# Kernel optimization log

Measured on AMD Instinct MI355X. Metric: run time of the kernel, lower is better.

The kernel has to match this reference:

```python
import jax, jax.numpy as jnp
import numpy as np
import math

B, S, E, H, DFF = 8, 1024, 1024, 16, 4096
DK = E // H
EPS = 1e-6


def _layernorm(x, alpha, bias):
    # Faithful to the torch module: uses unbiased std (ddof=1) and divides by (std + eps)
    mean = jnp.mean(x, axis=-1, keepdims=True)
    var = jnp.sum((x - mean) ** 2, axis=-1, keepdims=True) / (x.shape[-1] - 1)
    std = jnp.sqrt(var)
    return alpha * (x - mean) / (std + EPS) + bias


def setup_inputs() -> dict:
    key = jax.random.key(0)
    ks = jax.random.split(key, 16)
    sc_e = 1.0 / math.sqrt(E)
    sc_f = 1.0 / math.sqrt(DFF)
    inp = {
        "x": jax.random.normal(ks[0], (B, S, E), dtype=jnp.float32),
        "mask": jnp.ones((1, 1, S, S), dtype=jnp.int32),
        # linear weights stored as (in, out)
        "wq": jax.random.normal(ks[1], (E, E), jnp.float32) * sc_e,
        "bq": jnp.zeros((E,), jnp.float32),
        "wk": jax.random.normal(ks[2], (E, E), jnp.float32) * sc_e,
        "bk": jnp.zeros((E,), jnp.float32),
        "wv": jax.random.normal(ks[3], (E, E), jnp.float32) * sc_e,
        "bv": jnp.zeros((E,), jnp.float32),
        "wo": jax.random.normal(ks[4], (E, E), jnp.float32) * sc_e,
        "bo": jnp.zeros((E,), jnp.float32),
        "w1": jax.random.normal(ks[5], (E, DFF), jnp.float32) * sc_e,
        "b1": jnp.zeros((DFF,), jnp.float32),
        "w2": jax.random.normal(ks[6], (DFF, E), jnp.float32) * sc_f,
        "b2": jnp.zeros((E,), jnp.float32),
        "ln1_a": jnp.ones((E,), jnp.float32),
        "ln1_b": jnp.zeros((E,), jnp.float32),
        "ln2_a": jnp.ones((E,), jnp.float32),
        "ln2_b": jnp.zeros((E,), jnp.float32),
    }
    return inp


def _mha(x, mask, wq, bq, wk, bk, wv, bv, wo, bo):
    q = (x @ wq + bq).reshape(B, S, H, DK).transpose(0, 2, 1, 3)  # [B,H,S,DK]
    k = (x @ wk + bk).reshape(B, S, H, DK).transpose(0, 2, 1, 3)
    v = (x @ wv + bv).reshape(B, S, H, DK).transpose(0, 2, 1, 3)
    scores = jnp.einsum("bhqd,bhkd->bhqk", q, k) / math.sqrt(DK)  # [B,H,S,S]
    scores = jnp.where(mask == 0, jnp.float32(-1e9), scores)
    attn = jax.nn.softmax(scores, axis=-1)
    out = jnp.einsum("bhqk,bhkd->bhqd", attn, v)  # [B,H,S,DK]
    out = out.transpose(0, 2, 1, 3).reshape(B, S, E)
    return out @ wo + bo


def reference(x, mask, wq, bq, wk, bk, wv, bv, wo, bo, w1, b1, w2, b2,
              ln1_a, ln1_b, ln2_a, ln2_b):
    # Residual connection 1 (pre-norm): x + dropout(attn(norm(x))) ; dropout=0 at eval
    h1 = x + _mha(_layernorm(x, ln1_a, ln1_b), mask, wq, bq, wk, bk, wv, bv, wo, bo)
    # Residual connection 2: h1 + ffn(norm(h1))
    n2 = _layernorm(h1, ln2_a, ln2_b)
    ff = jax.nn.relu(n2 @ w1 + b1) @ w2 + b2
    return h1 + ff
```

## Files before the change

### kernel.cpp

```cpp
#include <hip/hip_runtime.h>
#include <hip/hip_bf16.h>
#include <cstdint>
#include <cstddef>

#define BB   8
#define SS   1024
#define EE   1024
#define HH   16
#define DKK  64
#define DFFN 4096
#define NROWS (BB*SS)

typedef __attribute__((ext_vector_type(8))) short short8;
typedef __attribute__((ext_vector_type(4))) short s16x4;
typedef __attribute__((ext_vector_type(4))) float f32x4;

__device__ __forceinline__ short f2bf(float f) {
  __hip_bfloat16 h = __float2bfloat16(f);
  return __builtin_bit_cast(short, h);
}

__device__ __forceinline__ void gload_lds16(const void* g, void* l) {
  __builtin_amdgcn_global_load_lds((const __attribute__((address_space(1))) void*)g,
                                   (__attribute__((address_space(3))) void*)l, 16, 0, 0);
}

__device__ __forceinline__ f32x4 mfma16(s16x4 a, s16x4 b, f32x4 c) {
#if __has_builtin(__builtin_amdgcn_mfma_f32_16x16x16_bf16)
  return __builtin_amdgcn_mfma_f32_16x16x16_bf16(a, b, c, 0, 0, 0);
#elif __has_builtin(__builtin_amdgcn_mfma_f32_16x16x16bf16_1k)
  return __builtin_amdgcn_mfma_f32_16x16x16bf16_1k(a, b, c, 0, 0, 0);
#else
  f32x4 d = c;
  asm("v_mfma_f32_16x16x16_bf16 %0, %1, %2, %0" : "+v"(d) : "v"(a), "v"(b));
  return d;
#endif
}

__global__ __launch_bounds__(256) void wtrans_kernel(const float* __restrict__ in,
                                                     short* __restrict__ out,
                                                     int R, int C) {
  __shared__ float tile[32][33];
  int c0 = blockIdx.x * 32, r0 = blockIdx.y * 32;
  int tx = threadIdx.x, ty = threadIdx.y;
#pragma unroll
  for (int i = 0; i < 32; i += 8)
    tile[ty + i][tx] = in[(size_t)(r0 + ty + i) * C + (c0 + tx)];
  __syncthreads();
#pragma unroll
  for (int i = 0; i < 32; i += 8)
    out[(size_t)(c0 + ty + i) * R + (r0 + tx)] = f2bf(tile[tx][ty + i]);
}

__global__ __launch_bounds__(256) void ln_kernel(const float* __restrict__ x,
                                                 const float* __restrict__ alpha,
                                                 const float* __restrict__ beta,
                                                 short* __restrict__ out) {
  __shared__ float sbuf[4];
  int row = blockIdx.x;
  int tid = threadIdx.x;
  const float* xr = x + (size_t)row * EE;
  float4 v = reinterpret_cast<const float4*>(xr)[tid];
  float s = v.x + v.y + v.z + v.w;
#pragma unroll
  for (int o = 32; o > 0; o >>= 1) s += __shfl_down(s, o);
  if ((tid & 63) == 0) sbuf[tid >> 6] = s;
  __syncthreads();
  float mean = (sbuf[0] + sbuf[1] + sbuf[2] + sbuf[3]) * (1.0f / EE);
  __syncthreads();
  float dx = v.x - mean, dy = v.y - mean, dz = v.z - mean, dw = v.w - mean;
  float sq = dx * dx + dy * dy + dz * dz + dw * dw;
#pragma unroll
  for (int o = 32; o > 0; o >>= 1) sq += __shfl_down(sq, o);
  if ((tid & 63) == 0) sbuf[tid >> 6] = sq;
  __syncthreads();
  float var = (sbuf[0] + sbuf[1] + sbuf[2] + sbuf[3]) * (1.0f / (EE - 1));
  float inv = 1.0f / (sqrtf(var) + 1e-6f);
  float4 a = reinterpret_cast<const float4*>(alpha)[tid];
  float4 b = reinterpret_cast<const float4*>(beta)[tid];
  size_t base = (size_t)row * EE + tid * 4;
  out[base + 0] = f2bf(a.x * dx * inv + b.x);
  out[base + 1] = f2bf(a.y * dy * inv + b.y);
  out[base + 2] = f2bf(a.z * dz * inv + b.z);
  out[base + 3] = f2bf(a.w * dw * inv + b.w);
}

template <int EPI>
__global__ __launch_bounds__(256, 4) void gemm_bt(const short* __restrict__ A,
                                                  const short* __restrict__ Bt,
                                                  const float* __restrict__ bias,
                                                  const float* __restrict__ resid,
                                                  void* __restrict__ out,
                                                  int N, int K, int NTN) {
  __shared__ short As[2][4096];
  __shared__ short Bs[2][4096];
  int tid = threadIdx.x;
  int lane = tid & 63, w = tid >> 6;
  int wr = w >> 1, wc = w & 1;
  int g = lane >> 4, c = lane & 15;

  int nwg = gridDim.x;
  int wg = blockIdx.x;
  int swg = (wg & 7) * (nwg >> 3) + (wg >> 3);
  int mt = swg / NTN, nt = swg % NTN;
  int m0 = mt * 128, n0 = nt * 128;

  int r0 = tid >> 2;
  int gslot = (tid & 3) ^ ((r0 >> 1) & 3);
  const short* pA = A + (size_t)(m0 + r0) * K + gslot * 8;
  const short* pB = Bt + (size_t)(n0 + r0) * K + gslot * 8;
  const size_t row64 = (size_t)64 * K;

  f32x4 acc[4][4] = {};

#define STAGE(B, T)                                                             \
  {                                                                             \
    gload_lds16(pA + (size_t)(T) * 32,         (char*)As[B] + w * 1024);        \
    gload_lds16(pA + (size_t)(T) * 32 + row64, (char*)As[B] + 4096 + w * 1024); \
    gload_lds16(pB + (size_t)(T) * 32,         (char*)Bs[B] + w * 1024);        \
    gload_lds16(pB + (size_t)(T) * 32 + row64, (char*)Bs[B] + 4096 + w * 1024); \
  }

  int NKT = K >> 5;
  STAGE(0, 0);
  __syncthreads();
  int buf = 0;

  int so = (g ^ ((c >> 1) & 3)) * 8;

  for (int t = 0; t < NKT; ++t) {
    if (t + 1 < NKT) STAGE(buf ^ 1, t + 1);

    short8 af[4], bfr[4];
#pragma unroll
    for (int i = 0; i < 4; ++i) {
      af[i]  = *(const short8*)&As[buf][(wr * 64 + i * 16 + c) * 32 + so];
      bfr[i] = *(const short8*)&Bs[buf][(wc * 64 + i * 16 + c) * 32 + so];
    }
    __builtin_amdgcn_s_setprio(1);
#pragma unroll
    for (int mi = 0; mi < 4; ++mi)
#pragma unroll
      for (int nf = 0; nf < 4; ++nf)
        acc[mi][nf] = __builtin_amdgcn_mfma_f32_16x16x32_bf16(af[mi], bfr[nf], acc[mi][nf], 0, 0, 0);
    __builtin_amdgcn_s_setprio(0);
    __syncthreads();
    buf ^= 1;
  }
#undef STAGE

  int rb_ = m0 + wr * 64;
  int cb_ = n0 + wc * 64;
#pragma unroll
  for (int mi = 0; mi < 4; ++mi) {
#pragma unroll
    for (int nf = 0; nf < 4; ++nf) {
      int col = cb_ + nf * 16 + c;
      float bv = bias[col];
      if (EPI == 5) {
        int which = col >> 10;
        int inner = col & 1023;
        int h = inner >> 6, d = inner & 63;
        if (which < 2) {
          short* dst = (short*)out + (size_t)which * (8u * 1024 * 1024);
#pragma unroll
          for (int j = 0; j < 4; ++j) {
            int row = rb_ + mi * 16 + g * 4 + j;
            int b = row >> 10, s = row & 1023;
            dst[(((size_t)(b * HH + h)) * SS + s) * DKK + d] = f2bf(acc[mi][nf][j] + bv);
          }
        } else {
          int row0 = rb_ + mi * 16 + g * 4;
          int b = row0 >> 10, s0 = row0 & 1023;
          s16x4 pkv;
#pragma unroll
          for (int j = 0; j < 4; ++j) pkv[j] = f2bf(acc[mi][nf][j] + bv);
          *(s16x4*)((short*)out + 2u * 8 * 1024 * 1024 +
                    (((size_t)(b * HH + h)) * DKK + d) * SS + s0) = pkv;
        }
      } else {
#pragma unroll
        for (int j = 0; j < 4; ++j) {
          int row = rb_ + mi * 16 + g * 4 + j;
          float val = acc[mi][nf][j] + bv;
          if (EPI == 1) {
            ((short*)out)[(size_t)row * N + col] = f2bf(val > 0.f ? val : 0.f);
          } else {
            ((float*)out)[(size_t)row * N + col] = resid[(size_t)row * N + col] + val;
          }
        }
      }
    }
  }
}

__global__ __launch_bounds__(256, 3) void attn_kernel(const short* __restrict__ q,
                                                      const short* __restrict__ k,
                                                      const short* __restrict__ vt,
                                                      short* __restrict__ out) {
  __shared__ short Ks[2][64 * 64];
  __shared__ short Vs[2][64 * 64];
  int bh = blockIdx.x, qt = blockIdx.y;
  int tid = threadIdx.x, lane = tid & 63, w = tid >> 6;
  int g = lane >> 4, c = lane & 15;
  const short* qp = q + (size_t)bh * SS * DKK;
  const short* kp = k + (size_t)bh * SS * DKK;
  const short* vp = vt + (size_t)bh * DKK * SS;

  int q0 = qt * 128 + w * 32;

  short8 qf[2][2];
#pragma unroll
  for (int qb = 0; qb < 2; ++qb)
#pragma unroll
    for (int ks = 0; ks < 2; ++ks)
      qf[qb][ks] = *(const short8*)(qp + (size_t)(q0 + qb * 16 + c) * DKK + ks * 32 + g * 8);

  f32x4 oacc[2][4];
#pragma unroll
  for (int qb = 0; qb < 2; ++qb)
#pragma unroll
    for (int nd = 0; nd < 4; ++nd)
#pragma unroll
      for (int j = 0; j < 4; ++j) oacc[qb][nd][j] = 0.f;
  float mrun[2] = {-1e30f, -1e30f}, lrun[2] = {0.f, 0.f};

  int rs = lane >> 3;
  int cs = lane & 7;
  int swz = (cs ^ rs) * 8;

  int buf = 0;
#define STAGE(B, T)                                                                  \
  {                                                                                  \
    _Pragma("unroll")                                                                \
    for (int cc = 0; cc < 2; ++cc) {                                                 \
      int chunk = w * 2 + cc;                                                        \
      int row = chunk * 8 + rs;                                                      \
      gload_lds16(kp + (size_t)((T) * 64 + row) * DKK + swz, &Ks[B][chunk * 512]);   \
      gload_lds16(vp + (size_t)row * SS + (T) * 64 + swz, &Vs[B][chunk * 512]);      \
    }                                                                                \
  }

  STAGE(0, 0);
  __syncthreads();

  for (int t = 0; t < SS / 64; ++t) {
    if (t < SS / 64 - 1) STAGE(buf ^ 1, t + 1);

    f32x4 sc[2][4];
#pragma unroll
    for (int qb = 0; qb < 2; ++qb)
#pragma unroll
      for (int nf = 0; nf < 4; ++nf)
#pragma unroll
        for (int j = 0; j < 4; ++j) sc[qb][nf][j] = 0.f;
#pragma unroll
    for (int ks = 0; ks < 2; ++ks) {
      short8 kf[4];
#pragma unroll
      for (int nf = 0; nf < 4; ++nf) {
        int row = nf * 16 + c;
        int off = row * 64 + (((ks * 64 + g * 16) ^ ((c & 7) << 4)) >> 1);
        kf[nf] = *(const short8*)&Ks[buf][off];
      }
#pragma unroll
      for (int qb = 0; qb < 2; ++qb)
#pragma unroll
        for (int nf = 0; nf < 4; ++nf)
          sc[qb][nf] = __builtin_amdgcn_mfma_f32_16x16x32_bf16(kf[nf], qf[qb][ks], sc[qb][nf], 0, 0, 0);
    }

    s16x4 pk[2][4];
    float corr[2];
#pragma unroll
    for (int qb = 0; qb < 2; ++qb) {
      float pm = -1e30f;
#pragma unroll
      for (int nf = 0; nf < 4; ++nf)
#pragma unroll
        for (int j = 0; j < 4; ++j) pm = fmaxf(pm, sc[qb][nf][j]);
      pm = fmaxf(pm, __shfl_xor(pm, 16));
      pm = fmaxf(pm, __shfl_xor(pm, 32));
      pm *= 0.125f;
      float mnew = fmaxf(mrun[qb], pm);
      corr[qb] = __expf(mrun[qb] - mnew);
      mrun[qb] = mnew;
      float rsum = 0.f;
#pragma unroll
      for (int nf = 0; nf < 4; ++nf) {
        float p0 = __expf(sc[qb][nf][0] * 0.125f - mnew);
        float p1 = __expf(sc[qb][nf][1] * 0.125f - mnew);
        float p2 = __expf(sc[qb][nf][2] * 0.125f - mnew);
        float p3 = __expf(sc[qb][nf][3] * 0.125f - mnew);
        rsum += (p0 + p1) + (p2 + p3);
        pk[qb][nf][0] = f2bf(p0); pk[qb][nf][1] = f2bf(p1);
        pk[qb][nf][2] = f2bf(p2); pk[qb][nf][3] = f2bf(p3);
      }
      rsum += __shfl_xor(rsum, 16);
      rsum += __shfl_xor(rsum, 32);
      lrun[qb] = lrun[qb] * corr[qb] + rsum;
    }
#pragma unroll
    for (int qb = 0; qb < 2; ++qb) {
      float cj[4];
#pragma unroll
      for (int j = 0; j < 4; ++j) cj[j] = __shfl(corr[qb], (lane & 48) | (g * 4 + j));
#pragma unroll
      for (int nd = 0; nd < 4; ++nd)
#pragma unroll
        for (int j = 0; j < 4; ++j) oacc[qb][nd][j] *= cj[j];
    }

#pragma unroll
    for (int nf = 0; nf < 4; ++nf) {
      s16x4 vf[4];
#pragma unroll
      for (int nd = 0; nd < 4; ++nd) {
        int row = nd * 16 + c;
        int off = row * 64 + (((nf * 32 + g * 8) ^ ((c & 7) << 4)) >> 1);
        vf[nd] = *(const s16x4*)&Vs[buf][off];
      }
#pragma unroll
      for (int qb = 0; qb < 2; ++qb)
#pragma unroll
        for (int nd = 0; nd < 4; ++nd)
          oacc[qb][nd] = mfma16(pk[qb][nf], vf[nd], oacc[qb][nd]);
    }
    __syncthreads();
    buf ^= 1;
  }
#undef STAGE

  int b = bh >> 4, h = bh & 15;
#pragma unroll
  for (int qb = 0; qb < 2; ++qb) {
#pragma unroll
    for (int j = 0; j < 4; ++j) {
      float linv = 1.0f / __shfl(lrun[qb], (lane & 48) | (g * 4 + j));
      int srow = q0 + qb * 16 + g * 4 + j;
#pragma unroll
      for (int nd = 0; nd < 4; ++nd)
        out[((size_t)b * SS + srow) * EE + h * DKK + nd * 16 + c] = f2bf(oacc[qb][nd][j] * linv);
    }
  }
}

extern "C" void kernel_launch(void* const* d_in, const int* in_sizes, int n_in,
                              void* d_out, int out_size, void* d_ws, size_t ws_size,
                              hipStream_t stream) {
  (void)in_sizes; (void)n_in; (void)out_size; (void)ws_size;
  const float* x   = (const float*)d_in[0];
  const float* wq  = (const float*)d_in[2];  const float* bq  = (const float*)d_in[3];
  const float* wk  = (const float*)d_in[4];  const float* bk  = (const float*)d_in[5];
  const float* wv  = (const float*)d_in[6];  const float* bv  = (const float*)d_in[7];
  const float* wo  = (const float*)d_in[8];  const float* bo  = (const float*)d_in[9];
  const float* w1  = (const float*)d_in[10]; const float* b1  = (const float*)d_in[11];
  const float* w2  = (const float*)d_in[12]; const float* b2  = (const float*)d_in[13];
  const float* l1a = (const float*)d_in[14]; const float* l1b = (const float*)d_in[15];
  const float* l2a = (const float*)d_in[16]; const float* l2b = (const float*)d_in[17];
  float* out = (float*)d_out;

  char* ws = (char*)d_ws;
  const size_t MB = 1024ull * 1024ull;
  short* wqkvT = (short*)(ws + 0 * MB);
  short* woT = (short*)(ws + 6 * MB);
  short* w1T = (short*)(ws + 8 * MB);
  short* w2T = (short*)(ws + 16 * MB);
  short* n1  = (short*)(ws + 24 * MB);
  short* qb  = (short*)(ws + 40 * MB);
  short* ff1 = (short*)(ws + 40 * MB);
  short* ao  = (short*)(ws + 88 * MB);
  float* bqkv = (float*)(ws + 100 * MB);
  float* h1  = (float*)(ws + 104 * MB);

  hipMemcpyAsync(bqkv,        bq, EE * sizeof(float), hipMemcpyDeviceToDevice, stream);
  hipMemcpyAsync(bqkv + EE,   bk, EE * sizeof(float), hipMemcpyDeviceToDevice, stream);
  hipMemcpyAsync(bqkv + 2*EE, bv, EE * sizeof(float), hipMemcpyDeviceToDevice, stream);

  dim3 tb(32, 8);
  wtrans_kernel<<<dim3(EE / 32, EE / 32), tb, 0, stream>>>(wq, wqkvT, EE, EE);
  wtrans_kernel<<<dim3(EE / 32, EE / 32), tb, 0, stream>>>(wk, wqkvT + 1024 * 1024, EE, EE);
  wtrans_kernel<<<dim3(EE / 32, EE / 32), tb, 0, stream>>>(wv, wqkvT + 2 * 1024 * 1024, EE, EE);
  wtrans_kernel<<<dim3(EE / 32, EE / 32), tb, 0, stream>>>(wo, woT, EE, EE);
  wtrans_kernel<<<dim3(DFFN / 32, EE / 32), tb, 0, stream>>>(w1, w1T, EE, DFFN);
  wtrans_kernel<<<dim3(EE / 32, DFFN / 32), tb, 0, stream>>>(w2, w2T, DFFN, EE);

  ln_kernel<<<NROWS, 256, 0, stream>>>(x, l1a, l1b, n1);

  gemm_bt<5><<<dim3(64 * 24), 256, 0, stream>>>(n1, wqkvT, bqkv, nullptr, qb, 3072, EE, 24);

  attn_kernel<<<dim3(BB * HH, SS / 128), 256, 0, stream>>>(qb, qb + 8 * 1024 * 1024,
                                                           qb + 16 * 1024 * 1024, ao);

  gemm_bt<2><<<dim3(64 * 8), 256, 0, stream>>>(ao, woT, bo, x, h1, EE, EE, 8);

  ln_kernel<<<NROWS, 256, 0, stream>>>(h1, l2a, l2b, n1);

  gemm_bt<1><<<dim3(64 * 32), 256, 0, stream>>>(n1, w1T, b1, nullptr, ff1, DFFN, EE, 32);
  gemm_bt<2><<<dim3(64 * 8), 256, 0, stream>>>(ff1, w2T, b2, h1, out, EE, DFFN, 8);
}
```

Baseline: 404.2 us.

## Triple-buffer GEMM LDS staging with manual waitcnt and one barrier per tile

Replaces the double-buffered LDS pipeline in the bf16 GEMM kernel with a three-slot ring. Two K tiles are prefetched ahead, and each iteration loads fragments from the current slot, issues the next global-to-LDS loads, then waits with explicit vmcnt/lgkmcnt counts and a single barrier before the MFMAs. The goal is to hide more global load latency behind compute and remove the trailing __syncthreads. In exchange it raises LDS use per block by half and lowers the launch-bounds occupancy hint from 4 to 3, which may reduce waves per CU.

```diff
diff --git a/kernel.cpp b/kernel.cpp
--- a/kernel.cpp
+++ b/kernel.cpp
@@ -86,14 +86,14 @@
 }
 
 template <int EPI>
-__global__ __launch_bounds__(256, 4) void gemm_bt(const short* __restrict__ A,
+__global__ __launch_bounds__(256, 3) void gemm_bt(const short* __restrict__ A,
                                                   const short* __restrict__ Bt,
                                                   const float* __restrict__ bias,
                                                   const float* __restrict__ resid,
                                                   void* __restrict__ out,
                                                   int N, int K, int NTN) {
-  __shared__ short As[2][4096];
-  __shared__ short Bs[2][4096];
+  __shared__ short As[3][4096];
+  __shared__ short Bs[3][4096];
   int tid = threadIdx.x;
   int lane = tid & 63, w = tid >> 6;
   int wr = w >> 1, wc = w & 1;
@@ -113,41 +113,72 @@
 
   f32x4 acc[4][4] = {};
 
-#define STAGE(B, T)                                                             \
-  {                                                                             \
-    gload_lds16(pA + (size_t)(T) * 32,         (char*)As[B] + w * 1024);        \
-    gload_lds16(pA + (size_t)(T) * 32 + row64, (char*)As[B] + 4096 + w * 1024); \
-    gload_lds16(pB + (size_t)(T) * 32,         (char*)Bs[B] + w * 1024);        \
-    gload_lds16(pB + (size_t)(T) * 32 + row64, (char*)Bs[B] + 4096 + w * 1024); \
+#define STAGE(SL, T)                                                                \
+  {                                                                                 \
+    gload_lds16(pA + (size_t)(T) * 32,         (char*)As[SL] + w * 1024);           \
+    gload_lds16(pA + (size_t)(T) * 32 + row64, (char*)As[SL] + 4096 + w * 1024);    \
+    gload_lds16(pB + (size_t)(T) * 32,         (char*)Bs[SL] + w * 1024);           \
+    gload_lds16(pB + (size_t)(T) * 32 + row64, (char*)Bs[SL] + 4096 + w * 1024);    \
+  }
+
+  int so = (g ^ ((c >> 1) & 3)) * 8;
+  int raA = (wr * 64 + c) * 32 + so;
+  int raB = (wc * 64 + c) * 32 + so;
+
+  short8 af[4], bfr[4];
+
+#define FRAGS(SL)                                                \
+  {                                                              \
+    _Pragma("unroll") for (int i = 0; i < 4; ++i) {              \
+      af[i]  = *(const short8*)&As[SL][raA + i * 512];           \
+      bfr[i] = *(const short8*)&Bs[SL][raB + i * 512];           \
+    }                                                            \
+  }
+
+#define MFMAS                                                                        \
+  {                                                                                  \
+    __builtin_amdgcn_s_setprio(1);                                                   \
+    _Pragma("unroll") for (int mi = 0; mi < 4; ++mi)                                 \
+        _Pragma("unroll") for (int nf = 0; nf < 4; ++nf)                             \
+            acc[mi][nf] = __builtin_amdgcn_mfma_f32_16x16x32_bf16(af[mi], bfr[nf],   \
+                                                                  acc[mi][nf], 0, 0, 0); \
+    __builtin_amdgcn_s_setprio(0);                                                   \
   }
 
   int NKT = K >> 5;
+
   STAGE(0, 0);
-  __syncthreads();
-  int buf = 0;
-
-  int so = (g ^ ((c >> 1) & 3)) * 8;
-
-  for (int t = 0; t < NKT; ++t) {
-    if (t + 1 < NKT) STAGE(buf ^ 1, t + 1);
-
-    short8 af[4], bfr[4];
-#pragma unroll
-    for (int i = 0; i < 4; ++i) {
-      af[i]  = *(const short8*)&As[buf][(wr * 64 + i * 16 + c) * 32 + so];
-      bfr[i] = *(const short8*)&Bs[buf][(wc * 64 + i * 16 + c) * 32 + so];
-    }
-    __builtin_amdgcn_s_setprio(1);
-#pragma unroll
-    for (int mi = 0; mi < 4; ++mi)
-#pragma unroll
-      for (int nf = 0; nf < 4; ++nf)
-        acc[mi][nf] = __builtin_amdgcn_mfma_f32_16x16x32_bf16(af[mi], bfr[nf], acc[mi][nf], 0, 0, 0);
-    __builtin_amdgcn_s_setprio(0);
-    __syncthreads();
-    buf ^= 1;
-  }
+  STAGE(1, 1);
+  asm volatile("s_waitcnt vmcnt(4)" ::: "memory");
+  __builtin_amdgcn_s_barrier();
+
+  int cur = 0;
+  for (int t = 0; t < NKT - 2; ++t) {
+    int nxt = cur + 2; if (nxt >= 3) nxt -= 3;
+    FRAGS(cur);
+    STAGE(nxt, t + 2);
+    asm volatile("s_waitcnt lgkmcnt(0)" ::: "memory");
+    asm volatile("s_waitcnt vmcnt(4)" ::: "memory");
+    __builtin_amdgcn_s_barrier();
+    __builtin_amdgcn_sched_barrier(0);
+    MFMAS;
+    ++cur; if (cur >= 3) cur -= 3;
+  }
+  FRAGS(cur);
+  asm volatile("s_waitcnt lgkmcnt(0)" ::: "memory");
+  asm volatile("s_waitcnt vmcnt(0)" ::: "memory");
+  __builtin_amdgcn_s_barrier();
+  __builtin_amdgcn_sched_barrier(0);
+  MFMAS;
+  ++cur; if (cur >= 3) cur -= 3;
+  FRAGS(cur);
+  asm volatile("s_waitcnt lgkmcnt(0)" ::: "memory");
+  __builtin_amdgcn_sched_barrier(0);
+  MFMAS;
+
 #undef STAGE
+#undef FRAGS
+#undef MFMAS
 
   int rb_ = m0 + wr * 64;
   int cb_ = n0 + wc * 64;
```

New measurement: 395.2 us. 2.2% less time.

## Add 256x256-tile 512-thread GEMM with phased LDS pipeline for QKV and FFN1

Applied to the files above, without the earlier changes.

Adds a new GEMM kernel that uses 256x256 output tiles, 8 waves, and 128KB of dynamic LDS. It double-buffers A and B and runs a four-phase schedule that interleaves the global-to-LDS loads with MFMA work under explicit barriers and waitcnts. The QKV projection and the first FFN GEMM switch to it, which raises operand reuse per byte loaded. In exchange there are fewer workgroups (384 and 512 on 256 CUs), more accumulator registers, and the 128KB LDS launch has to succeed. The old kernel's QKV epilogue is stripped.

```diff
diff --git a/kernel.cpp b/kernel.cpp
--- a/kernel.cpp
+++ b/kernel.cpp
@@ -83,6 +83,168 @@
   out[base + 1] = f2bf(a.y * dy * inv + b.y);
   out[base + 2] = f2bf(a.z * dz * inv + b.z);
   out[base + 3] = f2bf(a.w * dw * inv + b.w);
+}
+
+template <int EPI>
+__global__ __launch_bounds__(512, 2) void gemm256(const short* __restrict__ A,
+                                                  const short* __restrict__ Bt,
+                                                  const float* __restrict__ bias,
+                                                  const float* __restrict__ resid,
+                                                  void* __restrict__ out,
+                                                  int N, int K, int NTN) {
+  extern __shared__ char lds[];
+  int tid = threadIdx.x, lane = tid & 63, w = tid >> 6;
+  int wm = w >> 2, wn = w & 3;
+  int g = lane >> 4, c = lane & 15;
+
+  int nwg = gridDim.x, wg = blockIdx.x;
+  int swg = (wg & 7) * (nwg >> 3) + (wg >> 3);
+  int mt = swg / NTN, nt = swg % NTN;
+  int m0 = mt * 256, n0 = nt * 256;
+
+  int rS = tid >> 3;
+  int gslot = (tid & 7) ^ ((tid >> 4) & 7);
+  const short* pA = A + (size_t)(m0 + rS) * K + gslot * 8;
+  const short* pB = Bt + (size_t)(n0 + rS) * K + gslot * 8;
+
+#define STAGE_A(b, h, T)                                                                   \
+  {                                                                                        \
+    gload_lds16(pA + (size_t)((h)*128) * K + (size_t)(T)*64,                               \
+                lds + (b)*32768 + (h)*16384 + tid * 16);                                   \
+    gload_lds16(pA + (size_t)((h)*128 + 64) * K + (size_t)(T)*64,                          \
+                lds + (b)*32768 + (h)*16384 + 8192 + tid * 16);                            \
+  }
+#define STAGE_B(b, h, T)                                                                   \
+  {                                                                                        \
+    gload_lds16(pB + (size_t)((h)*128) * K + (size_t)(T)*64,                               \
+                lds + 65536 + (b)*32768 + (h)*16384 + tid * 16);                           \
+    gload_lds16(pB + (size_t)((h)*128 + 64) * K + (size_t)(T)*64,                          \
+                lds + 65536 + (b)*32768 + (h)*16384 + 8192 + tid * 16);                    \
+  }
+#define WAITV(NN) asm volatile("s_waitcnt vmcnt(" #NN ")" ::: "memory")
+
+  int aoff0 = ((0 * 4 + g) ^ (c >> 1)) * 16;
+  int aoff1 = ((1 * 4 + g) ^ (c >> 1)) * 16;
+  char* ldsAb = lds + (wm * 128 + c) * 128;
+  char* ldsBb = lds + 65536 + (wn * 64 + c) * 128;
+
+  f32x4 acc[8][4] = {};
+  short8 af[2][2], bfr[4][2];
+
+#define READB(b)                                                                           \
+  {                                                                                        \
+    _Pragma("unroll") for (int nf = 0; nf < 4; ++nf) {                                     \
+      bfr[nf][0] = *(const short8*)(ldsBb + (b)*32768 + nf * 2048 + aoff0);                \
+      bfr[nf][1] = *(const short8*)(ldsBb + (b)*32768 + nf * 2048 + aoff1);                \
+    }                                                                                      \
+  }
+
+#define PHASE(b, q, STAGEOP, ENDWAIT)                                                      \
+  {                                                                                        \
+    _Pragma("unroll") for (int mi = 0; mi < 2; ++mi) {                                     \
+      af[mi][0] = *(const short8*)(ldsAb + (b)*32768 + ((q)*32 + mi * 16) * 128 + aoff0);  \
+      af[mi][1] = *(const short8*)(ldsAb + (b)*32768 + ((q)*32 + mi * 16) * 128 + aoff1);  \
+    }                                                                                      \
+    STAGEOP;                                                                               \
+    __builtin_amdgcn_s_barrier();                                                          \
+    asm volatile("s_waitcnt lgkmcnt(0)" ::: "memory");                                     \
+    __builtin_amdgcn_sched_barrier(0);                                                     \
+    __builtin_amdgcn_s_setprio(1);                                                         \
+    _Pragma("unroll") for (int mi = 0; mi < 2; ++mi)                                       \
+      _Pragma("unroll") for (int nf = 0; nf < 4; ++nf) {                                   \
+        acc[(q)*2 + mi][nf] = __builtin_amdgcn_mfma_f32_16x16x32_bf16(                     \
+            af[mi][0], bfr[nf][0], acc[(q)*2 + mi][nf], 0, 0, 0);                          \
+        acc[(q)*2 + mi][nf] = __builtin_amdgcn_mfma_f32_16x16x32_bf16(                     \
+            af[mi][1], bfr[nf][1], acc[(q)*2 + mi][nf], 0, 0, 0);                          \
+      }                                                                                    \
+    __builtin_amdgcn_s_setprio(0);                                                         \
+    ENDWAIT;                                                                               \
+    __builtin_amdgcn_s_barrier();                                                          \
+  }
+
+  int NKT = K >> 6;
+
+  STAGE_A(0, 0, 0); STAGE_A(0, 1, 0);
+  STAGE_B(0, 0, 0); STAGE_B(0, 1, 0);
+  STAGE_B(1, 0, 1); STAGE_B(1, 1, 1);
+  WAITV(4);
+  __builtin_amdgcn_s_barrier();
+
+  for (int t = 0; t < NKT - 2; t += 2) {
+    READB(0);
+    PHASE(0, 0, STAGE_A(1, 0, t + 1), );
+    PHASE(0, 1, STAGE_A(1, 1, t + 1), );
+    PHASE(0, 2, STAGE_B(0, 0, t + 2), );
+    PHASE(0, 3, STAGE_B(0, 1, t + 2), WAITV(4));
+    READB(1);
+    PHASE(1, 0, STAGE_A(0, 0, t + 2), );
+    PHASE(1, 1, STAGE_A(0, 1, t + 2), );
+    PHASE(1, 2, STAGE_B(1, 0, t + 3), );
+    PHASE(1, 3, STAGE_B(1, 1, t + 3), WAITV(4));
+  }
+  {
+    int t = NKT - 2;
+    READB(0);
+    PHASE(0, 0, STAGE_A(1, 0, t + 1), );
+    PHASE(0, 1, STAGE_A(1, 1, t + 1), );
+    PHASE(0, 2, , );
+    PHASE(0, 3, , WAITV(0));
+    READB(1);
+    PHASE(1, 0, , );
+    PHASE(1, 1, , );
+    PHASE(1, 2, , );
+    PHASE(1, 3, , );
+  }
+
+#undef STAGE_A
+#undef STAGE_B
+#undef READB
+#undef PHASE
+#undef WAITV
+
+  int rb_ = m0 + wm * 128;
+  int cb_ = n0 + wn * 64;
+#pragma unroll
+  for (int fm = 0; fm < 8; ++fm) {
+#pragma unroll
+    for (int nf = 0; nf < 4; ++nf) {
+      int col = cb_ + nf * 16 + c;
+      float bv = bias[col];
+      if (EPI == 5) {
+        int which = col >> 10;
+        int inner = col & 1023;
+        int h = inner >> 6, d = inner & 63;
+        if (which < 2) {
+          short* dst = (short*)out + (size_t)which * (8u * 1024 * 1024);
+#pragma unroll
+          for (int j = 0; j < 4; ++j) {
+            int row = rb_ + fm * 16 + g * 4 + j;
+            int b = row >> 10, s = row & 1023;
+            dst[(((size_t)(b * HH + h)) * SS + s) * DKK + d] = f2bf(acc[fm][nf][j] + bv);
+          }
+        } else {
+          int row0 = rb_ + fm * 16 + g * 4;
+          int b = row0 >> 10, s0 = row0 & 1023;
+          s16x4 pkv;
+#pragma unroll
+          for (int j = 0; j < 4; ++j) pkv[j] = f2bf(acc[fm][nf][j] + bv);
+          *(s16x4*)((short*)out + 2u * 8 * 1024 * 1024 +
+                    (((size_t)(b * HH + h)) * DKK + d) * SS + s0) = pkv;
+        }
+      } else {
+#pragma unroll
+        for (int j = 0; j < 4; ++j) {
+          int row = rb_ + fm * 16 + g * 4 + j;
+          float val = acc[fm][nf][j] + bv;
+          if (EPI == 1) {
+            ((short*)out)[(size_t)row * N + col] = f2bf(val > 0.f ? val : 0.f);
+          } else {
+            ((float*)out)[(size_t)row * N + col] = resid[(size_t)row * N + col] + val;
+          }
+        }
+      }
+    }
+  }
 }
 
 template <int EPI>
@@ -157,37 +319,14 @@
     for (int nf = 0; nf < 4; ++nf) {
       int col = cb_ + nf * 16 + c;
       float bv = bias[col];
-      if (EPI == 5) {
-        int which = col >> 10;
-        int inner = col & 1023;
-        int h = inner >> 6, d = inner & 63;
-        if (which < 2) {
-          short* dst = (short*)out + (size_t)which * (8u * 1024 * 1024);
-#pragma unroll
-          for (int j = 0; j < 4; ++j) {
-            int row = rb_ + mi * 16 + g * 4 + j;
-            int b = row >> 10, s = row & 1023;
-            dst[(((size_t)(b * HH + h)) * SS + s) * DKK + d] = f2bf(acc[mi][nf][j] + bv);
-          }
+#pragma unroll
+      for (int j = 0; j < 4; ++j) {
+        int row = rb_ + mi * 16 + g * 4 + j;
+        float val = acc[mi][nf][j] + bv;
+        if (EPI == 1) {
+          ((short*)out)[(size_t)row * N + col] = f2bf(val > 0.f ? val : 0.f);
         } else {
-          int row0 = rb_ + mi * 16 + g * 4;
-          int b = row0 >> 10, s0 = row0 & 1023;
-          s16x4 pkv;
-#pragma unroll
-          for (int j = 0; j < 4; ++j) pkv[j] = f2bf(acc[mi][nf][j] + bv);
-          *(s16x4*)((short*)out + 2u * 8 * 1024 * 1024 +
-                    (((size_t)(b * HH + h)) * DKK + d) * SS + s0) = pkv;
-        }
-      } else {
-#pragma unroll
-        for (int j = 0; j < 4; ++j) {
-          int row = rb_ + mi * 16 + g * 4 + j;
-          float val = acc[mi][nf][j] + bv;
-          if (EPI == 1) {
-            ((short*)out)[(size_t)row * N + col] = f2bf(val > 0.f ? val : 0.f);
-          } else {
-            ((float*)out)[(size_t)row * N + col] = resid[(size_t)row * N + col] + val;
-          }
+          ((float*)out)[(size_t)row * N + col] = resid[(size_t)row * N + col] + val;
         }
       }
     }
@@ -387,7 +526,7 @@
 
   ln_kernel<<<NROWS, 256, 0, stream>>>(x, l1a, l1b, n1);
 
-  gemm_bt<5><<<dim3(64 * 24), 256, 0, stream>>>(n1, wqkvT, bqkv, nullptr, qb, 3072, EE, 24);
+  gemm256<5><<<dim3(32 * 12), 512, 131072, stream>>>(n1, wqkvT, bqkv, nullptr, qb, 3072, EE, 12);
 
   attn_kernel<<<dim3(BB * HH, SS / 128), 256, 0, stream>>>(qb, qb + 8 * 1024 * 1024,
                                                            qb + 16 * 1024 * 1024, ao);
@@ -396,6 +535,6 @@
 
   ln_kernel<<<NROWS, 256, 0, stream>>>(h1, l2a, l2b, n1);
 
-  gemm_bt<1><<<dim3(64 * 32), 256, 0, stream>>>(n1, w1T, b1, nullptr, ff1, DFFN, EE, 32);
+  gemm256<1><<<dim3(32 * 16), 512, 131072, stream>>>(n1, w1T, b1, nullptr, ff1, DFFN, EE, 16);
   gemm_bt<2><<<dim3(64 * 8), 256, 0, stream>>>(ff1, w2T, b2, h1, out, EE, DFFN, 8);
 }
```

After: 385.2 us. 4.7% less time.
